# Kernel tuning notes

Measured on AMD Instinct MI355X. Metric: run time of the kernel, lower is better.

## Reference

```python
import jax, jax.numpy as jnp
import numpy as np

LMBDA = 100.0
GAMMA = 0.5
EPS_EV = 1e-10


def _safe_evals(e):
    return jnp.clip(jnp.nan_to_num(e, nan=EPS_EV, posinf=1e6, neginf=EPS_EV), EPS_EV, None)


def get_mask(evals1, evals2, gamma):
    # evals1, evals2: [B, K]; returns D: [B, K, K] with D[b,i,j] from (evals2[b,i], evals1[b,j])
    e1 = _safe_evals(evals1)
    e2 = _safe_evals(evals2)
    scale = jnp.clip(jnp.maximum(e1.max(axis=1), e2.max(axis=1)), 1e-10, None)[:, None]
    e1 = e1 / scale
    e2 = e2 / scale
    g1 = e1 ** gamma  # [B,K] -> broadcast as column index j
    g2 = e2 ** gamma  # [B,K] -> broadcast as row index i
    d1 = g1 * g1 + 1.0
    d2 = g2 * g2 + 1.0
    M_re = (g2 / d2)[:, :, None] - (g1 / d1)[:, None, :]
    M_im = (1.0 / d2)[:, :, None] - (1.0 / d1)[:, None, :]
    return jnp.nan_to_num(M_re * M_re + M_im * M_im, nan=0.0, posinf=1e6, neginf=0.0)


def setup_inputs() -> dict:
    key = jax.random.key(0)
    k = jax.random.split(key, 6)
    B, N, K, C = 8, 20000, 128, 256
    return {
        "feat_x": jax.random.normal(k[0], (B, N, C), dtype=jnp.float32),
        "feat_y": jax.random.normal(k[1], (B, N, C), dtype=jnp.float32),
        "evals_x": jax.random.uniform(k[2], (B, K), dtype=jnp.float32),
        "evals_y": jax.random.uniform(k[3], (B, K), dtype=jnp.float32),
        "evecs_trans_x": jax.random.normal(k[4], (B, K, N), dtype=jnp.float32),
        "evecs_trans_y": jax.random.normal(k[5], (B, K, N), dtype=jnp.float32),
    }


def reference(feat_x, feat_y, evals_x, evals_y, evecs_trans_x, evecs_trans_y):
    # Spectral projection of features: [B,K,N] @ [B,N,C] -> [B,K,C]
    A = jnp.einsum('bkn,bnc->bkc', evecs_trans_x, feat_x)
    Bm = jnp.einsum('bkn,bnc->bkc', evecs_trans_y, feat_y)
    D = get_mask(evals_x, evals_y, GAMMA)  # [B,K,K]

    A_A_t = jnp.einsum('bic,bjc->bij', A, A)   # [B,K,K]
    B_A_t = jnp.einsum('bic,bjc->bij', Bm, A)  # [B,K,K]

    K = A.shape[1]
    eye = jnp.eye(K, dtype=A.dtype)
    # lhs[b,i] = A_A_t[b] + lmbda * diag(D[b,i]) + 1e-8 * I  -> [B,K,K,K]
    lhs = A_A_t[:, None, :, :] + LMBDA * (D[..., None] * eye) + 1e-8 * eye
    rhs = B_A_t[..., None]  # [B,K,K,1]; rhs[b,i] = B_A_t[b,i,:]
    Cxy = jnp.linalg.solve(lhs, rhs)[..., 0]  # [B,K,K]; row i of Cxy = solution for eigenvalue i
    return Cxy
```

## Files before the change

### kernel.cpp

```cpp
#include <hip/hip_runtime.h>
#include <math.h>

#define B_ 8
#define N_ 20000
#define K_ 128
#define C_ 256

static_assert(N_ % 32 == 0, "N must be multiple of 32");

constexpr float LMBDA = 100.0f;
constexpr float EPS_EV = 1e-10f;

typedef unsigned int u32x4 __attribute__((ext_vector_type(4)));
typedef short short8_t __attribute__((ext_vector_type(8)));
typedef float f32x4 __attribute__((ext_vector_type(4)));

static __device__ inline void split2(float x0, float x1, unsigned& h, unsigned& l) {
  unsigned u0 = __builtin_bit_cast(unsigned, x0);
  unsigned u1 = __builtin_bit_cast(unsigned, x1);
  h = __builtin_amdgcn_perm(u1, u0, 0x07060302u);
  float r0 = x0 - __builtin_bit_cast(float, u0 & 0xFFFF0000u);
  float r1 = x1 - __builtin_bit_cast(float, u1 & 0xFFFF0000u);
  unsigned v0 = __builtin_bit_cast(unsigned, r0);
  unsigned v1 = __builtin_bit_cast(unsigned, r1);
  v0 += 0x7FFFu + ((v0 >> 16) & 1u);
  v1 += 0x7FFFu + ((v1 >> 16) & 1u);
  l = __builtin_amdgcn_perm(v1, v0, 0x07060302u);
}

#define KFENCE()                                              \
  do {                                                        \
    asm volatile("s_waitcnt lgkmcnt(0)" ::: "memory");        \
    __builtin_amdgcn_sched_barrier(0);                        \
    __builtin_amdgcn_s_barrier();                             \
    __builtin_amdgcn_sched_barrier(0);                        \
  } while (0)

__global__ __launch_bounds__(512, 4)
void proj_mfma(const float* __restrict__ feat_x, const float* __restrict__ feat_y,
               const float* __restrict__ evx, const float* __restrict__ evy,
               float* __restrict__ part, int Sa, int chunk) {
  const int bm = blockIdx.z;
  const int b = bm >> 1, mat = bm & 1;
  const float* __restrict__ E = (mat ? evy : evx) + (size_t)b * K_ * N_;
  const float* __restrict__ F = (mat ? feat_y : feat_x) + (size_t)b * N_ * C_;
  const int c0 = blockIdx.x << 7;
  const int s = blockIdx.y;
  const int nb = s * chunk;
  const int ne = min(N_, nb + chunk);
  const int nt = (ne - nb) >> 5;

  __shared__ unsigned short Ah[2][128][40];
  __shared__ unsigned short Al[2][128][40];
  __shared__ unsigned short Bh[2][128][40];
  __shared__ unsigned short Bl[2][128][40];

  const int t = threadIdx.x;
  const int lane = t & 63, wv = t >> 6;
  const int wm = wv & 3;
  const int wcc = wv >> 2;
  const int lr = lane & 15, lg = lane >> 4;

  const int am = t >> 2, ak = (t & 3) << 3;
  const int cl = t & 127, gq = (t >> 7) << 2;
  const int sigw = ((cl >> 3) & 3) << 1;
  const int slotA = ((gq >> 2) ^ sigw) << 2;
  const int slotB = (((gq >> 2) + 4) ^ sigw) << 2;

  f32x4 acc[2][4];
#pragma unroll
  for (int i = 0; i < 2; ++i)
#pragma unroll
    for (int j = 0; j < 4; ++j) acc[i][j] = (f32x4){0.f, 0.f, 0.f, 0.f};

  struct Stage { float4 a0, a1; float b0, b1, b2, b3, b4, b5, b6, b7; };

  auto LOAD = [&](Stage& st, int n0) {
    const float* ep = E + (size_t)am * N_ + n0 + ak;
    st.a0 = *(const float4*)ep;
    st.a1 = *(const float4*)(ep + 4);
    const float* fp = F + (size_t)(n0 + gq) * C_ + c0 + cl;
    st.b0 = fp[0];
    st.b1 = fp[C_];
    st.b2 = fp[2 * C_];
    st.b3 = fp[3 * C_];
    const float* fp2 = fp + (size_t)16 * C_;
    st.b4 = fp2[0];
    st.b5 = fp2[C_];
    st.b6 = fp2[2 * C_];
    st.b7 = fp2[3 * C_];
  };

  auto WRITE = [&](Stage& st, int p) {
    unsigned h01, l01, h23, l23, h45, l45, h67, l67;
    split2(st.a0.x, st.a0.y, h01, l01);
    split2(st.a0.z, st.a0.w, h23, l23);
    split2(st.a1.x, st.a1.y, h45, l45);
    split2(st.a1.z, st.a1.w, h67, l67);
    *(u32x4*)&Ah[p][am][ak] = (u32x4){h01, h23, h45, h67};
    *(u32x4*)&Al[p][am][ak] = (u32x4){l01, l23, l45, l67};
    split2(st.b0, st.b1, h01, l01);
    split2(st.b2, st.b3, h23, l23);
    *(uint2*)&Bh[p][cl][slotA] = (uint2){h01, h23};
    *(uint2*)&Bl[p][cl][slotA] = (uint2){l01, l23};
    split2(st.b4, st.b5, h45, l45);
    split2(st.b6, st.b7, h67, l67);
    *(uint2*)&Bh[p][cl][slotB] = (uint2){h45, h67};
    *(uint2*)&Bl[p][cl][slotB] = (uint2){l45, l67};
  };

  auto COMPUTE = [&](int p) {
    const int k0 = lg << 3;
    short8_t a_h[2], a_l[2];
#pragma unroll
    for (int mt = 0; mt < 2; ++mt) {
      const int m = (wm << 5) + (mt << 4) + lr;
      a_h[mt] = *(const short8_t*)&Ah[p][m][k0];
      a_l[mt] = *(const short8_t*)&Al[p][m][k0];
    }
#pragma unroll
    for (int ct = 0; ct < 4; ++ct) {
      const int c = (wcc << 6) + (ct << 4) + lr;
      const int sig = ((c >> 3) & 3) << 1;
      const int koff = (((lg << 1) ^ sig)) << 2;
      const short8_t b_h = *(const short8_t*)&Bh[p][c][koff];
      const short8_t b_l = *(const short8_t*)&Bl[p][c][koff];
#pragma unroll
      for (int mt = 0; mt < 2; ++mt) {
        acc[mt][ct] = __builtin_amdgcn_mfma_f32_16x16x32_bf16(a_h[mt], b_h, acc[mt][ct], 0, 0, 0);
        acc[mt][ct] = __builtin_amdgcn_mfma_f32_16x16x32_bf16(a_l[mt], b_h, acc[mt][ct], 0, 0, 0);
        acc[mt][ct] = __builtin_amdgcn_mfma_f32_16x16x32_bf16(a_h[mt], b_l, acc[mt][ct], 0, 0, 0);
      }
    }
  };

  Stage sA, sB;
  LOAD(sA, nb);
  if (nt > 1) LOAD(sB, nb + 32);
  WRITE(sA, 0);
  KFENCE();

  for (int it = 0; it < nt; it += 2) {
    if (it + 1 < nt) WRITE(sB, 1);
    if (it + 2 < nt) LOAD(sA, nb + ((it + 2) << 5));
    COMPUTE(0);
    KFENCE();
    if (it + 1 < nt) {
      if (it + 2 < nt) WRITE(sA, 0);
      if (it + 3 < nt) LOAD(sB, nb + ((it + 3) << 5));
      COMPUTE(1);
      KFENCE();
    }
  }

  float* __restrict__ P = part + ((size_t)bm * Sa + s) * (K_ * C_);
#pragma unroll
  for (int mt = 0; mt < 2; ++mt)
#pragma unroll
    for (int ct = 0; ct < 4; ++ct) {
      const int ccol = c0 + (wcc << 6) + (ct << 4) + lr;
#pragma unroll
      for (int r = 0; r < 4; ++r) {
        const int mrow = (wm << 5) + (mt << 4) + (lg << 2) + r;
        P[(size_t)mrow * C_ + ccol] = acc[mt][ct][r];
      }
    }
}

__global__ void reduce_parts(const float* __restrict__ part, float* __restrict__ AB, int Sa) {
  const int idx4 = blockIdx.x * 256 + threadIdx.x;
  if (idx4 >= 16 * K_ * C_ / 4) return;
  const int per = K_ * C_ / 4;
  const int bm = idx4 / per;
  const int rem4 = idx4 - bm * per;
  float4 v = {0.f, 0.f, 0.f, 0.f};
  for (int s = 0; s < Sa; ++s) {
    const float4 p = *(const float4*)&part[((size_t)bm * Sa + s) * (K_ * C_) + rem4 * 4];
    v.x += p.x; v.y += p.y; v.z += p.z; v.w += p.w;
  }
  *(float4*)&AB[(size_t)idx4 * 4] = v;
}

__global__ __launch_bounds__(256)
void gram_kernel(const float* __restrict__ AB, float* __restrict__ Sm, float* __restrict__ Rm) {
  const int b = blockIdx.x, which = blockIdx.y, qz = blockIdx.z;
  const int iq = (qz & 1) << 6, jq = (qz >> 1) << 6;
  const float* __restrict__ L  = AB + ((size_t)(b * 2 + which)) * (K_ * C_);
  const float* __restrict__ Ar = AB + ((size_t)(b * 2)) * (K_ * C_);
  float* __restrict__ out = (which ? Rm : Sm) + (size_t)b * (K_ * K_);
  const int t = threadIdx.x;
  const int ir = iq + ((t >> 4) << 2), jc = jq + ((t & 15) << 2);
  float acc[4][4] = {};
  for (int c0 = 0; c0 < C_; c0 += 4) {
    float4 li[4], rj[4];
#pragma unroll
    for (int i = 0; i < 4; ++i) li[i] = *(const float4*)(L + (size_t)(ir + i) * C_ + c0);
#pragma unroll
    for (int j = 0; j < 4; ++j) rj[j] = *(const float4*)(Ar + (size_t)(jc + j) * C_ + c0);
#pragma unroll
    for (int i = 0; i < 4; ++i)
#pragma unroll
      for (int j = 0; j < 4; ++j)
        acc[i][j] += li[i].x * rj[j].x + li[i].y * rj[j].y +
                     li[i].z * rj[j].z + li[i].w * rj[j].w;
  }
#pragma unroll
  for (int i = 0; i < 4; ++i)
#pragma unroll
    for (int j = 0; j < 4; ++j) {
      float v = acc[i][j];
      if (!which && (ir + i) == (jc + j)) v += 1e-8f;
      out[(size_t)(ir + i) * K_ + (jc + j)] = v;
    }
}

__global__ void mask_prep(const float* __restrict__ evx, const float* __restrict__ evy,
                          float* __restrict__ PQ) {
  const int b = blockIdx.x, t = threadIdx.x;
  float e1 = evx[b * K_ + t];
  float e2 = evy[b * K_ + t];
  if (e1 != e1) e1 = EPS_EV;
  if (e2 != e2) e2 = EPS_EV;
  e1 = fminf(fmaxf(e1, EPS_EV), 1e6f);
  e2 = fminf(fmaxf(e2, EPS_EV), 1e6f);

  __shared__ float wmax[2];
  float v = fmaxf(e1, e2);
#pragma unroll
  for (int d = 1; d < 64; d <<= 1) v = fmaxf(v, __shfl_xor(v, d, 64));
  if ((t & 63) == 0) wmax[t >> 6] = v;
  __syncthreads();
  const float scale = fmaxf(fmaxf(wmax[0], wmax[1]), 1e-10f);

  const float g1 = sqrtf(e1 / scale);
  const float g2 = sqrtf(e2 / scale);
  const float d1 = fmaf(g1, g1, 1.f);
  const float d2 = fmaf(g2, g2, 1.f);
  float* P = PQ + b * 512;
  P[t]       = g1 / d1;
  P[128 + t] = 1.f / d1;
  P[256 + t] = g2 / d2;
  P[384 + t] = 1.f / d2;
}

__global__ __launch_bounds__(512)
void gj_inverse(const float* __restrict__ Sm, float* __restrict__ Sinv) {
  const int b = blockIdx.x, t = threadIdx.x;
  __shared__ float a[K_ * 132];
  __shared__ float Pi[16 * 20];
  __shared__ float Rp[16 * 132];
  __shared__ float Cp[K_ * 20];
  const float* __restrict__ Sb = Sm + (size_t)b * (K_ * K_);
#pragma unroll
  for (int l = 0; l < 8; ++l) {
    int f = t + (l << 9);
    int i = f >> 5, j = (f & 31) << 2;
    *(float4*)&a[i * 132 + j] = *(const float4*)(Sb + i * K_ + j);
  }
  __syncthreads();

  const int j = t & 127, rr = t >> 7;
  const int lane = t & 63;

  for (int p = 0; p < 8; ++p) {
    const int pb = p << 4;

    if (t < 64) {
      const int r = lane & 15, g = lane >> 4;
      float4 v4 = *(const float4*)&a[(pb + r) * 132 + pb + (g << 2)];
      float vv[4] = {v4.x, v4.y, v4.z, v4.w};
#pragma unroll
      for (int k = 0; k < 16; ++k) {
        const int srcrow = (lane & 48) | k;
        float rk[4];
        rk[0] = __shfl(vv[0], srcrow);
        rk[1] = __shfl(vv[1], srcrow);
        rk[2] = __shfl(vv[2], srcrow);
        rk[3] = __shfl(vv[3], srcrow);
        const int kg = (k >> 2) << 4;
        const float pv = __shfl(vv[k & 3], kg | k);
        const float c  = __shfl(vv[k & 3], kg | r);
        const float pr = 1.0f / pv;
        float rs[4];
#pragma unroll
        for (int e = 0; e < 4; ++e) rs[e] = rk[e] * pr;
        if (r == k) {
#pragma unroll
          for (int e = 0; e < 4; ++e) vv[e] = rs[e];
          if (g == (k >> 2)) vv[k & 3] = pr;
        } else {
#pragma unroll
          for (int e = 0; e < 4; ++e) vv[e] = fmaf(-c, rs[e], vv[e]);
          if (g == (k >> 2)) vv[k & 3] = -c * pr;
        }
      }
      Pi[r * 20 + (g << 2) + 0] = vv[0];
      Pi[r * 20 + (g << 2) + 1] = vv[1];
      Pi[r * 20 + (g << 2) + 2] = vv[2];
      Pi[r * 20 + (g << 2) + 3] = vv[3];
    }
    __syncthreads();

    {
      float Ak[16];
#pragma unroll
      for (int k = 0; k < 16; ++k) Ak[k] = a[(pb + k) * 132 + j];
      const unsigned jj = (unsigned)(j - pb);
      const int r0 = rr << 2;
#pragma unroll
      for (int q = 0; q < 4; ++q) {
        const int r = r0 + q;
        float acc = 0.f;
#pragma unroll
        for (int k = 0; k < 16; ++k) acc = fmaf(Pi[r * 20 + k], Ak[k], acc);
        Rp[r * 132 + j] = (jj < 16u) ? Pi[r * 20 + jj] : acc;
      }
      const int i = j;
      const int cb = rr << 2;
      float4 cA = *(const float4*)&a[i * 132 + pb + cb];
      *(float4*)&Cp[i * 20 + cb] = cA;
    }
    __syncthreads();

    {
      float Rk[16];
#pragma unroll
      for (int k = 0; k < 16; ++k) Rk[k] = Rp[k * 132 + j];
      const unsigned jj = (unsigned)(j - pb);
      const int i0 = rr << 5;
#pragma unroll 4
      for (int m = 0; m < 32; ++m) {
        const int i = i0 + m;
        const float4 c0 = *(const float4*)&Cp[i * 20];
        const float4 c1 = *(const float4*)&Cp[i * 20 + 4];
        const float4 c2 = *(const float4*)&Cp[i * 20 + 8];
        const float4 c3 = *(const float4*)&Cp[i * 20 + 12];
        float u0 = c0.x * Rk[0] + c0.y * Rk[1] + c0.z * Rk[2] + c0.w * Rk[3];
        float u1 = c1.x * Rk[4] + c1.y * Rk[5] + c1.z * Rk[6] + c1.w * Rk[7];
        float u2 = c2.x * Rk[8] + c2.y * Rk[9] + c2.z * Rk[10] + c2.w * Rk[11];
        float u3 = c3.x * Rk[12] + c3.y * Rk[13] + c3.z * Rk[14] + c3.w * Rk[15];
        const float upd = (u0 + u1) + (u2 + u3);
        const unsigned ii = (unsigned)(i - pb);
        float newv;
        if (ii < 16u) {
          newv = Rk[ii];
        } else {
          const float base = (jj < 16u) ? 0.f : a[i * 132 + j];
          newv = base - upd;
        }
        a[i * 132 + j] = newv;
      }
    }
    __syncthreads();
  }

  float* __restrict__ O = Sinv + (size_t)b * (K_ * K_);
#pragma unroll
  for (int l = 0; l < 8; ++l) {
    int f = t + (l << 9);
    int i = f >> 5, jq = (f & 31) << 2;
    *(float4*)(O + i * K_ + jq) = *(const float4*)&a[i * 132 + jq];
  }
}

__global__ __launch_bounds__(256)
void solve_iter(const float* __restrict__ Rm, const float* __restrict__ Sinv,
                const float* __restrict__ PQ, const float* __restrict__ Xin,
                float* __restrict__ Xout, const int first) {
  const int bb = blockIdx.x;
  const int b = bb >> 2, rb = (bb & 3) << 5;
  const int t = threadIdx.x;
  __shared__ float Tt[32][34];
  __shared__ float Sv[32][132];
  __shared__ float q1[K_], p1[K_], q2l[32], p2l[32];
  {
    const float* P = PQ + b * 512;
    if (t < K_) { q1[t] = P[t]; p1[t] = P[128 + t]; }
    if (t < 32) { q2l[t] = P[256 + rb + t]; p2l[t] = P[384 + rb + t]; }
  }
  __syncthreads();
  const float* __restrict__ Rb = Rm + (size_t)b * (K_ * K_);
  const float* __restrict__ Xb = Xin + (size_t)b * (K_ * K_);
  const float* __restrict__ Si = Sinv + (size_t)b * (K_ * K_);
  const int ir = (t >> 4) << 1, jc = (t & 15) << 3;
  float acc[2][8] = {};

  for (int k0 = 0; k0 < K_; k0 += 32) {
    {
      const int i = t >> 3;
      const int kk = (t & 7) << 2;
      const int k = k0 + kk;
      const int gi = rb + i;
      float4 tv = *(const float4*)(Rb + (size_t)gi * K_ + k);
      if (!first) {
        const float4 x4 = *(const float4*)(Xb + (size_t)gi * K_ + k);
        const float qi = q2l[i], pi = p2l[i];
        float dq, dp, w;
        dq = qi - q1[k + 0]; dp = pi - p1[k + 0]; w = fmaf(dq, dq, dp * dp);
        tv.x = fmaf(-LMBDA * w, x4.x, tv.x);
        dq = qi - q1[k + 1]; dp = pi - p1[k + 1]; w = fmaf(dq, dq, dp * dp);
        tv.y = fmaf(-LMBDA * w, x4.y, tv.y);
        dq = qi - q1[k + 2]; dp = pi - p1[k + 2]; w = fmaf(dq, dq, dp * dp);
        tv.z = fmaf(-LMBDA * w, x4.z, tv.z);
        dq = qi - q1[k + 3]; dp = pi - p1[k + 3]; w = fmaf(dq, dq, dp * dp);
        tv.w = fmaf(-LMBDA * w, x4.w, tv.w);
      }
      Tt[kk + 0][i] = tv.x; Tt[kk + 1][i] = tv.y;
      Tt[kk + 2][i] = tv.z; Tt[kk + 3][i] = tv.w;
    }
#pragma unroll
    for (int l = 0; l < 4; ++l) {
      int f = t + (l << 8);
      int kk = f >> 5, j4 = (f & 31) << 2;
      *(float4*)&Sv[kk][j4] = *(const float4*)(Si + (size_t)(k0 + kk) * K_ + j4);
    }
    __syncthreads();
#pragma unroll
    for (int kk = 0; kk < 32; ++kk) {
      const float2 a2 = *(const float2*)&Tt[kk][ir];
      const float4 b0 = *(const float4*)&Sv[kk][jc];
      const float4 b1 = *(const float4*)&Sv[kk][jc + 4];
      const float bv[8] = {b0.x, b0.y, b0.z, b0.w, b1.x, b1.y, b1.z, b1.w};
#pragma unroll
      for (int jx = 0; jx < 8; ++jx) {
        acc[0][jx] = fmaf(a2.x, bv[jx], acc[0][jx]);
        acc[1][jx] = fmaf(a2.y, bv[jx], acc[1][jx]);
      }
    }
    __syncthreads();
  }

  float* __restrict__ O = Xout + (size_t)b * (K_ * K_);
#pragma unroll
  for (int i = 0; i < 2; ++i) {
    float4 o0 = {acc[i][0], acc[i][1], acc[i][2], acc[i][3]};
    float4 o1 = {acc[i][4], acc[i][5], acc[i][6], acc[i][7]};
    *(float4*)(O + (size_t)(rb + ir + i) * K_ + jc) = o0;
    *(float4*)(O + (size_t)(rb + ir + i) * K_ + jc + 4) = o1;
  }
}

extern "C" void kernel_launch(void* const* d_in, const int* in_sizes, int n_in,
                              void* d_out, int out_size, void* d_ws, size_t ws_size,
                              hipStream_t stream) {
  (void)in_sizes; (void)n_in; (void)out_size;
  const float* feat_x  = (const float*)d_in[0];
  const float* feat_y  = (const float*)d_in[1];
  const float* evals_x = (const float*)d_in[2];
  const float* evals_y = (const float*)d_in[3];
  const float* evtx    = (const float*)d_in[4];
  const float* evty    = (const float*)d_in[5];
  float* out = (float*)d_out;
  float* ws  = (float*)d_ws;

  const size_t KC16 = (size_t)16 * K_ * C_;
  const size_t KK   = (size_t)K_ * K_;
  const size_t fixed = KC16 + 3 * (KK * B_) + 4096 + 2 * (KK * B_);
  const int T = N_ / 32;

  int S = 16, Sa = 16, chunk = 0;
  for (;;) {
    int steps = (T + S - 1) / S;
    chunk = steps * 32;
    Sa = (T + steps - 1) / steps;
    if (((size_t)Sa * KC16 + fixed) * sizeof(float) <= ws_size || S == 1) break;
    S >>= 1;
  }

  float* part = ws;
  float* AB   = part + (size_t)Sa * KC16;
  float* Sm   = AB + KC16;
  float* Rm   = Sm + KK * B_;
  float* Sinv = Rm + KK * B_;
  float* PQ   = Sinv + KK * B_;
  float* X0   = PQ + 4096;
  float* X1   = X0 + KK * B_;

  mask_prep<<<dim3(8), 128, 0, stream>>>(evals_x, evals_y, PQ);
  proj_mfma<<<dim3(2, Sa, 16), 512, 0, stream>>>(feat_x, feat_y, evtx, evty, part, Sa, chunk);
  reduce_parts<<<dim3(16 * K_ * C_ / 4 / 256), 256, 0, stream>>>(part, AB, Sa);
  gram_kernel<<<dim3(8, 2, 4), 256, 0, stream>>>(AB, Sm, Rm);
  gj_inverse<<<dim3(8), 512, 0, stream>>>(Sm, Sinv);
  solve_iter<<<dim3(32), 256, 0, stream>>>(Rm, Sinv, PQ, X0, X0, 1);
  solve_iter<<<dim3(32), 256, 0, stream>>>(Rm, Sinv, PQ, X0, X1, 0);
  solve_iter<<<dim3(32), 256, 0, stream>>>(Rm, Sinv, PQ, X1, out, 0);
}
```

Before: 254.2 us.

## Load A fragments directly into registers and shrink projection tile to 64 columns

The projection GEMM now has each wave load its eigenvector rows straight from global memory into MFMA operand registers, splitting them to bf16 hi/lo in registers and skipping the shared-memory A tiles. Only the feature (B) tile is staged in LDS, in a pre-swizzled layout that each lane reads directly. Blocks shrink to 256 threads covering 64 columns, so the grid doubles in x. This cuts LDS traffic and footprint, which may allow more resident blocks. The cost is that the eigenvector matrix is re-read from global memory by twice as many column blocks, and register pressure rises.

```diff
diff --git a/kernel.cpp b/kernel.cpp
--- a/kernel.cpp
+++ b/kernel.cpp
@@ -36,7 +36,7 @@
     __builtin_amdgcn_sched_barrier(0);                        \
   } while (0)
 
-__global__ __launch_bounds__(512, 4)
+__global__ __launch_bounds__(256, 4)
 void proj_mfma(const float* __restrict__ feat_x, const float* __restrict__ feat_y,
                const float* __restrict__ evx, const float* __restrict__ evy,
                float* __restrict__ part, int Sa, int chunk) {
@@ -44,28 +44,26 @@
   const int b = bm >> 1, mat = bm & 1;
   const float* __restrict__ E = (mat ? evy : evx) + (size_t)b * K_ * N_;
   const float* __restrict__ F = (mat ? feat_y : feat_x) + (size_t)b * N_ * C_;
-  const int c0 = blockIdx.x << 7;
+  const int c0 = blockIdx.x << 6;
   const int s = blockIdx.y;
   const int nb = s * chunk;
   const int ne = min(N_, nb + chunk);
   const int nt = (ne - nb) >> 5;
 
-  __shared__ unsigned short Ah[2][128][40];
-  __shared__ unsigned short Al[2][128][40];
-  __shared__ unsigned short Bh[2][128][40];
-  __shared__ unsigned short Bl[2][128][40];
+  __shared__ unsigned int BhL[2][1024];
+  __shared__ unsigned int BlL[2][1024];
 
   const int t = threadIdx.x;
-  const int lane = t & 63, wv = t >> 6;
-  const int wm = wv & 3;
-  const int wcc = wv >> 2;
+  const int lane = t & 63;
+  const int wm = t >> 6;
   const int lr = lane & 15, lg = lane >> 4;
 
-  const int am = t >> 2, ak = (t & 3) << 3;
-  const int cl = t & 127, gq = (t >> 7) << 2;
-  const int sigw = ((cl >> 3) & 3) << 1;
-  const int slotA = ((gq >> 2) ^ sigw) << 2;
-  const int slotB = (((gq >> 2) + 4) ^ sigw) << 2;
+  const int cl = lane;
+  const int g = wm;
+  const int slot4 = (((cl >> 4) << 6) + (g << 4) + (cl & 15)) << 2;
+
+  const size_t arow = (size_t)((wm << 5) + lr) * N_;
+  const int kofs = lg << 3;
 
   f32x4 acc[2][4];
 #pragma unroll
@@ -73,82 +71,77 @@
 #pragma unroll
     for (int j = 0; j < 4; ++j) acc[i][j] = (f32x4){0.f, 0.f, 0.f, 0.f};
 
-  struct Stage { float4 a0, a1; float b0, b1, b2, b3, b4, b5, b6, b7; };
-
-  auto LOAD = [&](Stage& st, int n0) {
-    const float* ep = E + (size_t)am * N_ + n0 + ak;
-    st.a0 = *(const float4*)ep;
-    st.a1 = *(const float4*)(ep + 4);
-    const float* fp = F + (size_t)(n0 + gq) * C_ + c0 + cl;
-    st.b0 = fp[0];
-    st.b1 = fp[C_];
-    st.b2 = fp[2 * C_];
-    st.b3 = fp[3 * C_];
-    const float* fp2 = fp + (size_t)16 * C_;
-    st.b4 = fp2[0];
-    st.b5 = fp2[C_];
-    st.b6 = fp2[2 * C_];
-    st.b7 = fp2[3 * C_];
+  float4 PAe[4], PAo[4];
+  float PBe[8], PBo[8];
+  u32x4 a_h[2], a_l[2];
+
+  auto LOADA = [&](float4* pa, int n0) {
+    const float* ep = E + arow + n0 + kofs;
+    pa[0] = *(const float4*)ep;
+    pa[1] = *(const float4*)(ep + 4);
+    const float* ep2 = ep + (size_t)16 * N_;
+    pa[2] = *(const float4*)ep2;
+    pa[3] = *(const float4*)(ep2 + 4);
   };
-
-  auto WRITE = [&](Stage& st, int p) {
-    unsigned h01, l01, h23, l23, h45, l45, h67, l67;
-    split2(st.a0.x, st.a0.y, h01, l01);
-    split2(st.a0.z, st.a0.w, h23, l23);
-    split2(st.a1.x, st.a1.y, h45, l45);
-    split2(st.a1.z, st.a1.w, h67, l67);
-    *(u32x4*)&Ah[p][am][ak] = (u32x4){h01, h23, h45, h67};
-    *(u32x4*)&Al[p][am][ak] = (u32x4){l01, l23, l45, l67};
-    split2(st.b0, st.b1, h01, l01);
-    split2(st.b2, st.b3, h23, l23);
-    *(uint2*)&Bh[p][cl][slotA] = (uint2){h01, h23};
-    *(uint2*)&Bl[p][cl][slotA] = (uint2){l01, l23};
-    split2(st.b4, st.b5, h45, l45);
-    split2(st.b6, st.b7, h67, l67);
-    *(uint2*)&Bh[p][cl][slotB] = (uint2){h45, h67};
-    *(uint2*)&Bl[p][cl][slotB] = (uint2){l45, l67};
+  auto LOADB = [&](float* pb, int n0) {
+    const float* fp = F + (size_t)(n0 + (g << 3)) * C_ + c0 + cl;
+#pragma unroll
+    for (int j = 0; j < 8; ++j) pb[j] = fp[(size_t)j * C_];
   };
-
+  auto SPLITA = [&](const float4* pa) {
+#pragma unroll
+    for (int mt = 0; mt < 2; ++mt) {
+      unsigned h0, l0, h1, l1, h2, l2, h3, l3;
+      split2(pa[2 * mt].x, pa[2 * mt].y, h0, l0);
+      split2(pa[2 * mt].z, pa[2 * mt].w, h1, l1);
+      split2(pa[2 * mt + 1].x, pa[2 * mt + 1].y, h2, l2);
+      split2(pa[2 * mt + 1].z, pa[2 * mt + 1].w, h3, l3);
+      a_h[mt] = (u32x4){h0, h1, h2, h3};
+      a_l[mt] = (u32x4){l0, l1, l2, l3};
+    }
+  };
+  auto WRITEB = [&](int p, const float* pb) {
+    unsigned h0, l0, h1, l1, h2, l2, h3, l3;
+    split2(pb[0], pb[1], h0, l0);
+    split2(pb[2], pb[3], h1, l1);
+    split2(pb[4], pb[5], h2, l2);
+    split2(pb[6], pb[7], h3, l3);
+    *(u32x4*)&BhL[p][slot4] = (u32x4){h0, h1, h2, h3};
+    *(u32x4*)&BlL[p][slot4] = (u32x4){l0, l1, l2, l3};
+  };
   auto COMPUTE = [&](int p) {
-    const int k0 = lg << 3;
-    short8_t a_h[2], a_l[2];
-#pragma unroll
-    for (int mt = 0; mt < 2; ++mt) {
-      const int m = (wm << 5) + (mt << 4) + lr;
-      a_h[mt] = *(const short8_t*)&Ah[p][m][k0];
-      a_l[mt] = *(const short8_t*)&Al[p][m][k0];
-    }
 #pragma unroll
     for (int ct = 0; ct < 4; ++ct) {
-      const int c = (wcc << 6) + (ct << 4) + lr;
-      const int sig = ((c >> 3) & 3) << 1;
-      const int koff = (((lg << 1) ^ sig)) << 2;
-      const short8_t b_h = *(const short8_t*)&Bh[p][c][koff];
-      const short8_t b_l = *(const short8_t*)&Bl[p][c][koff];
+      const short8_t b_h = *(const short8_t*)&BhL[p][(ct << 8) + (lane << 2)];
+      const short8_t b_l = *(const short8_t*)&BlL[p][(ct << 8) + (lane << 2)];
 #pragma unroll
       for (int mt = 0; mt < 2; ++mt) {
-        acc[mt][ct] = __builtin_amdgcn_mfma_f32_16x16x32_bf16(a_h[mt], b_h, acc[mt][ct], 0, 0, 0);
-        acc[mt][ct] = __builtin_amdgcn_mfma_f32_16x16x32_bf16(a_l[mt], b_h, acc[mt][ct], 0, 0, 0);
-        acc[mt][ct] = __builtin_amdgcn_mfma_f32_16x16x32_bf16(a_h[mt], b_l, acc[mt][ct], 0, 0, 0);
+        const short8_t ah = __builtin_bit_cast(short8_t, a_h[mt]);
+        const short8_t al = __builtin_bit_cast(short8_t, a_l[mt]);
+        acc[mt][ct] = __builtin_amdgcn_mfma_f32_16x16x32_bf16(ah, b_h, acc[mt][ct], 0, 0, 0);
+        acc[mt][ct] = __builtin_amdgcn_mfma_f32_16x16x32_bf16(al, b_h, acc[mt][ct], 0, 0, 0);
+        acc[mt][ct] = __builtin_amdgcn_mfma_f32_16x16x32_bf16(ah, b_l, acc[mt][ct], 0, 0, 0);
       }
     }
   };
 
-  Stage sA, sB;
-  LOAD(sA, nb);
-  if (nt > 1) LOAD(sB, nb + 32);
-  WRITE(sA, 0);
+  LOADA(PAe, nb); LOADB(PBe, nb);
+  if (nt > 1) { LOADA(PAo, nb + 32); LOADB(PBo, nb + 32); }
+  WRITEB(0, PBe);
+  SPLITA(PAe);
   KFENCE();
 
   for (int it = 0; it < nt; it += 2) {
-    if (it + 1 < nt) WRITE(sB, 1);
-    if (it + 2 < nt) LOAD(sA, nb + ((it + 2) << 5));
+    if (it + 1 < nt) WRITEB(1, PBo);
+    if (it + 2 < nt) { LOADA(PAe, nb + ((it + 2) << 5)); LOADB(PBe, nb + ((it + 2) << 5)); }
     COMPUTE(0);
+    if (it + 1 < nt) SPLITA(PAo);
     KFENCE();
     if (it + 1 < nt) {
-      if (it + 2 < nt) WRITE(sA, 0);
-      if (it + 3 < nt) LOAD(sB, nb + ((it + 3) << 5));
+      if (it + 2 < nt) WRITEB(0, PBe);
+      if (it + 3 < nt) { LOADA(PAo, nb + ((it + 3) << 5)); LOADB(PBo, nb + ((it + 3) << 5)); }
       COMPUTE(1);
+      if (it + 2 < nt) SPLITA(PAe);
       KFENCE();
     }
   }
@@ -158,7 +151,7 @@
   for (int mt = 0; mt < 2; ++mt)
 #pragma unroll
     for (int ct = 0; ct < 4; ++ct) {
-      const int ccol = c0 + (wcc << 6) + (ct << 4) + lr;
+      const int ccol = c0 + (ct << 4) + lr;
 #pragma unroll
       for (int r = 0; r < 4; ++r) {
         const int mrow = (wm << 5) + (mt << 4) + (lg << 2) + r;
@@ -477,7 +470,7 @@
   float* X1   = X0 + KK * B_;
 
   mask_prep<<<dim3(8), 128, 0, stream>>>(evals_x, evals_y, PQ);
-  proj_mfma<<<dim3(2, Sa, 16), 512, 0, stream>>>(feat_x, feat_y, evtx, evty, part, Sa, chunk);
+  proj_mfma<<<dim3(4, Sa, 16), 256, 0, stream>>>(feat_x, feat_y, evtx, evty, part, Sa, chunk);
   reduce_parts<<<dim3(16 * K_ * C_ / 4 / 256), 256, 0, stream>>>(part, AB, Sa);
   gram_kernel<<<dim3(8, 2, 4), 256, 0, stream>>>(AB, Sm, Rm);
   gj_inverse<<<dim3(8), 512, 0, stream>>>(Sm, Sinv);
```

Measured after the change: 294.7 us. 1.16x slower.
